# Kernel tuning notes

Hardware: AMD Instinct MI355X
Metric: run time of the kernel (lower is better)

The kernel has to match this reference:

```python
import jax, jax.numpy as jnp
import numpy as np

N_BINS = 15  # matches init n_bins; bin b covers (b/15, (b+1)/15]


def setup_inputs() -> dict:
    key = jax.random.key(0)
    k1, k2 = jax.random.split(key)
    N, C = 500000, 100
    logits = jax.random.normal(k1, (N, C), dtype=jnp.float32)
    labels = jax.random.randint(k2, (N,), 0, C)
    return {"logits": logits, "labels": labels}


def reference(logits, labels):
    n_bins = N_BINS
    N, C = logits.shape  # num_classes = labels.max()+1 == C w.h.p. for this data
    p = jax.nn.softmax(logits, axis=1)  # [N, C] class confidences
    # Original bin test: p > lower and p <= upper with boundaries linspace(0,1,n_bins+1)
    # => bin index = ceil(p * n_bins) - 1 (exact boundary values fall in the lower bin).
    bin_idx = jnp.clip(jnp.ceil(p * n_bins).astype(jnp.int32) - 1, 0, n_bins - 1)  # [N, C]
    # Flatten to a single segmented histogram over class*n_bins + bin.
    seg = (jnp.arange(C, dtype=jnp.int32)[None, :] * n_bins + bin_idx).reshape(-1)  # [N*C]
    conf = p.reshape(-1)
    correct = (labels[:, None] == jnp.arange(C)[None, :]).astype(p.dtype).reshape(-1)
    num_seg = C * n_bins
    cnt = jax.ops.segment_sum(jnp.ones_like(conf), seg, num_segments=num_seg)
    conf_sum = jax.ops.segment_sum(conf, seg, num_segments=num_seg)
    acc_sum = jax.ops.segment_sum(correct, seg, num_segments=num_seg)
    safe_cnt = jnp.maximum(cnt, 1.0)
    gap = jnp.abs(conf_sum / safe_cnt - acc_sum / safe_cnt)  # |avg_conf - acc| per (class,bin)
    prop = cnt / N  # prop_in_bin (each class column has N entries)
    per_bin = jnp.where(cnt > 0, gap * prop, 0.0)
    per_class_sce = per_bin.reshape(C, n_bins).sum(axis=1)  # [C]
    return per_class_sce.mean()
```

## Files before the change

### kernel.cpp

```cpp
#include <hip/hip_runtime.h>
#include <math.h>

#define NBINS 15
#define NCLS  100
#define NHALF 50
#define NSEG  (NBINS * NCLS)
#define R     4

template <int CTRL>
__device__ __forceinline__ float dpp_add_f32(float x) {
    int y = __builtin_amdgcn_update_dpp(0, __float_as_int(x), CTRL, 0xf, 0xf, true);
    return x + __int_as_float(y);
}
__device__ __forceinline__ float wave_sum64(float x) {
    x = dpp_add_f32<0x111>(x);
    x = dpp_add_f32<0x112>(x);
    x = dpp_add_f32<0x114>(x);
    x = dpp_add_f32<0x118>(x);
    x = dpp_add_f32<0x142>(x);
    x = dpp_add_f32<0x143>(x);
    return __int_as_float(__builtin_amdgcn_readlane(__float_as_int(x), 63));
}

__global__ __launch_bounds__(1024, 8)
void ece_hist(const float* __restrict__ logits,
              const int* __restrict__ labels,
              int N,
              double* __restrict__ g_conf,
              unsigned int* __restrict__ g_acc)
{
    __shared__ float        s_conf[NSEG];
    __shared__ unsigned int s_acc[NSEG];

    const int tid = threadIdx.x;
    for (int i = tid; i < NSEG; i += 1024) { s_conf[i] = 0.0f; s_acc[i] = 0u; }
    __syncthreads();

    const int  lane = tid & 63;
    const int  wv   = (blockIdx.x << 4) + (tid >> 6);
    const int  nwv  = gridDim.x << 4;
    const bool act  = lane < NHALF;

    float        conf0_a = 0.0f, conf0_b = 0.0f;
    unsigned int acc0_a  = 0u,   acc0_b  = 0u;

    const float2* base2 = reinterpret_cast<const float2*>(logits);

    for (int row0 = wv * R; row0 < N; row0 += nwv * R) {
        const bool full = (row0 + R <= N);
        float e0[R], e1[R], s[R];
        int   lbl[R];

        const float2* rp = base2 + (size_t)row0 * NHALF + lane;
        if (full) {
            #pragma unroll
            for (int r = 0; r < R; ++r) {
                float2 v = act ? rp[r * NHALF] : make_float2(0.0f, 0.0f);
                e0[r] = v.x; e1[r] = v.y;
            }
            int4 lb = *reinterpret_cast<const int4*>(labels + row0);
            lbl[0] = lb.x; lbl[1] = lb.y; lbl[2] = lb.z; lbl[3] = lb.w;
        } else {
            #pragma unroll
            for (int r = 0; r < R; ++r) {
                int row = min(row0 + r, N - 1);
                float2 v = act ? base2[(size_t)row * NHALF + lane] : make_float2(0.0f, 0.0f);
                e0[r] = v.x; e1[r] = v.y;
                lbl[r] = labels[row];
            }
        }

        #pragma unroll
        for (int r = 0; r < R; ++r) {
            e0[r] = act ? __expf(e0[r]) : 0.0f;
            e1[r] = act ? __expf(e1[r]) : 0.0f;
        }

        #pragma unroll
        for (int r = 0; r < R; ++r) s[r] = wave_sum64(e0[r] + e1[r]);

        #pragma unroll
        for (int r = 0; r < R; ++r) {
            if (!full && row0 + r >= N) break;
            const float inv    = __builtin_amdgcn_rcpf(s[r]);
            const float thresh = s[r] * (1.0f / (float)NBINS);
            const int   lb     = lbl[r];
            const bool  mine   = (lane == (lb >> 1));
            const int   lbbit  = lb & 1;

            {
                float p0 = e0[r] * inv;
                if (e0[r] > thresh) {
                    int b0 = min((int)ceilf(p0 * (float)NBINS) - 1, NBINS - 1);
                    atomicAdd(&s_conf[(2 * lane) * NBINS + b0], p0);
                    if (mine && lbbit == 0) atomicAdd(&s_acc[(2 * lane) * NBINS + b0], 1u);
                } else {
                    conf0_a += p0;
                    if (mine && lbbit == 0) ++acc0_a;
                }
            }
            {
                float p1 = e1[r] * inv;
                if (e1[r] > thresh) {
                    int b1 = min((int)ceilf(p1 * (float)NBINS) - 1, NBINS - 1);
                    atomicAdd(&s_conf[(2 * lane + 1) * NBINS + b1], p1);
                    if (mine && lbbit == 1) atomicAdd(&s_acc[(2 * lane + 1) * NBINS + b1], 1u);
                } else {
                    conf0_b += p1;
                    if (mine && lbbit == 1) ++acc0_b;
                }
            }
        }
    }

    if (act) {
        atomicAdd(&s_conf[(2 * lane) * NBINS], conf0_a);
        if (acc0_a) atomicAdd(&s_acc[(2 * lane) * NBINS], acc0_a);
        atomicAdd(&s_conf[(2 * lane + 1) * NBINS], conf0_b);
        if (acc0_b) atomicAdd(&s_acc[(2 * lane + 1) * NBINS], acc0_b);
    }

    __syncthreads();
    const int rot = (blockIdx.x * 61) % NSEG;
    for (int i = tid; i < NSEG; i += 1024) {
        int j = i + rot; if (j >= NSEG) j -= NSEG;
        float        c = s_conf[j];
        unsigned int a = s_acc[j];
        if (c != 0.0f) atomicAdd(&g_conf[j], (double)c);
        if (a)         atomicAdd(&g_acc[j], a);
    }
}

__global__ void ece_final(const double* __restrict__ g_conf,
                          const unsigned int* __restrict__ g_acc,
                          float* __restrict__ out, double inv_nc)
{
    __shared__ double sh[16];
    double t = 0.0;
    for (int i = threadIdx.x; i < NSEG; i += blockDim.x)
        t += fabs(g_conf[i] - (double)g_acc[i]);
    #pragma unroll
    for (int off = 32; off; off >>= 1) t += __shfl_xor(t, off);
    const int lane = threadIdx.x & 63, w = threadIdx.x >> 6;
    if (lane == 0) sh[w] = t;
    __syncthreads();
    if (threadIdx.x == 0) {
        double tot = 0.0;
        const int nw = (int)(blockDim.x >> 6);
        for (int i = 0; i < nw; ++i) tot += sh[i];
        out[0] = (float)(tot * inv_nc);
    }
}

extern "C" void kernel_launch(void* const* d_in, const int* in_sizes, int n_in,
                              void* d_out, int out_size, void* d_ws, size_t ws_size,
                              hipStream_t stream)
{
    const float* logits = (const float*)d_in[0];
    const int*   labels = (const int*)d_in[1];
    const int N = in_sizes[1];

    double*       g_conf = (double*)d_ws;
    unsigned int* g_acc  = (unsigned int*)(g_conf + NSEG);

    (void)hipMemsetAsync(d_ws, 0, NSEG * sizeof(double) + NSEG * sizeof(unsigned int), stream);

    ece_hist<<<512, 1024, 0, stream>>>(logits, labels, N, g_conf, g_acc);

    const double inv_nc = 1.0 / ((double)N * (double)NCLS);
    ece_final<<<1, 256, 0, stream>>>(g_conf, g_acc, (float*)d_out, inv_nc);
}
```

Baseline: 58.73 us.

## Fuse final reduction via last-block counter and prefetch next row tile

Merges the separate finalize kernel into the histogram kernel, using a global done counter so the last block computes the final sum. The main loop now software-prefetches the next tile of logits and labels into registers while processing the current one, to hide global load latency. The bin-0 accumulation is restructured to be branchless, and the atomic path is skipped when neither element is rare. In exchange it raises register pressure from double-buffering and adds a threadfence plus a global atomic per block.

```diff
diff --git a/kernel.cpp b/kernel.cpp
--- a/kernel.cpp
+++ b/kernel.cpp
@@ -6,6 +6,8 @@
 #define NHALF 50
 #define NSEG  (NBINS * NCLS)
 #define R     4
+#define NBLK  512
+#define NTHR  1024
 
 template <int CTRL>
 __device__ __forceinline__ float dpp_add_f32(float x) {
@@ -22,18 +24,42 @@
     return __int_as_float(__builtin_amdgcn_readlane(__float_as_int(x), 63));
 }
 
-__global__ __launch_bounds__(1024, 8)
-void ece_hist(const float* __restrict__ logits,
-              const int* __restrict__ labels,
-              int N,
-              double* __restrict__ g_conf,
-              unsigned int* __restrict__ g_acc)
+__device__ __forceinline__ void load_tile(const float2* __restrict__ base2,
+                                          const int* __restrict__ labels,
+                                          int r0, int N, bool act, int lane,
+                                          float2 (&b)[R], int (&lb)[R])
+{
+    if (r0 + R <= N) {
+        const float2* rp = base2 + (size_t)r0 * NHALF + lane;
+        #pragma unroll
+        for (int r = 0; r < R; ++r)
+            b[r] = act ? rp[r * NHALF] : make_float2(0.0f, 0.0f);
+        const int4 l4 = *reinterpret_cast<const int4*>(labels + r0);
+        lb[0] = l4.x; lb[1] = l4.y; lb[2] = l4.z; lb[3] = l4.w;
+    } else {
+        #pragma unroll
+        for (int r = 0; r < R; ++r) {
+            int row = min(r0 + r, N - 1);
+            b[r] = act ? base2[(size_t)row * NHALF + lane] : make_float2(0.0f, 0.0f);
+            lb[r] = labels[row];
+        }
+    }
+}
+
+__global__ __launch_bounds__(NTHR, 8)
+void ece_fused(const float* __restrict__ logits,
+               const int* __restrict__ labels,
+               int N,
+               double* __restrict__ g_conf,
+               unsigned int* __restrict__ g_acc,
+               unsigned int* __restrict__ g_done,
+               float* __restrict__ out, double inv_nc)
 {
     __shared__ float        s_conf[NSEG];
     __shared__ unsigned int s_acc[NSEG];
 
     const int tid = threadIdx.x;
-    for (int i = tid; i < NSEG; i += 1024) { s_conf[i] = 0.0f; s_acc[i] = 0u; }
+    for (int i = tid; i < NSEG; i += NTHR) { s_conf[i] = 0.0f; s_acc[i] = 0u; }
     __syncthreads();
 
     const int  lane = tid & 63;
@@ -44,73 +70,67 @@
     float        conf0_a = 0.0f, conf0_b = 0.0f;
     unsigned int acc0_a  = 0u,   acc0_b  = 0u;
 
-    const float2* base2 = reinterpret_cast<const float2*>(logits);
+    const float2* base2  = reinterpret_cast<const float2*>(logits);
+    const int     stride = nwv * R;
 
-    for (int row0 = wv * R; row0 < N; row0 += nwv * R) {
-        const bool full = (row0 + R <= N);
-        float e0[R], e1[R], s[R];
-        int   lbl[R];
+    int row0 = wv * R;
+    float2 cbuf[R]; int clbl[R];
+    if (row0 < N) load_tile(base2, labels, row0, N, act, lane, cbuf, clbl);
 
-        const float2* rp = base2 + (size_t)row0 * NHALF + lane;
-        if (full) {
-            #pragma unroll
-            for (int r = 0; r < R; ++r) {
-                float2 v = act ? rp[r * NHALF] : make_float2(0.0f, 0.0f);
-                e0[r] = v.x; e1[r] = v.y;
-            }
-            int4 lb = *reinterpret_cast<const int4*>(labels + row0);
-            lbl[0] = lb.x; lbl[1] = lb.y; lbl[2] = lb.z; lbl[3] = lb.w;
-        } else {
-            #pragma unroll
-            for (int r = 0; r < R; ++r) {
-                int row = min(row0 + r, N - 1);
-                float2 v = act ? base2[(size_t)row * NHALF + lane] : make_float2(0.0f, 0.0f);
-                e0[r] = v.x; e1[r] = v.y;
-                lbl[r] = labels[row];
-            }
+    while (row0 < N) {
+        const int nrow0 = row0 + stride;
+        float2 nbuf[R]; int nlbl[R];
+        if (nrow0 < N)
+            load_tile(base2, labels, nrow0, N, act, lane, nbuf, nlbl);
+
+        float e0[R], e1[R], s[R], invv[R], th[R];
+        #pragma unroll
+        for (int r = 0; r < R; ++r) {
+            e0[r] = act ? __expf(cbuf[r].x) : 0.0f;
+            e1[r] = act ? __expf(cbuf[r].y) : 0.0f;
+        }
+        #pragma unroll
+        for (int r = 0; r < R; ++r) s[r] = wave_sum64(e0[r] + e1[r]);
+        #pragma unroll
+        for (int r = 0; r < R; ++r) {
+            invv[r] = __builtin_amdgcn_rcpf(s[r]);
+            th[r]   = s[r] * (1.0f / (float)NBINS);
         }
 
         #pragma unroll
         for (int r = 0; r < R; ++r) {
-            e0[r] = act ? __expf(e0[r]) : 0.0f;
-            e1[r] = act ? __expf(e1[r]) : 0.0f;
-        }
-
-        #pragma unroll
-        for (int r = 0; r < R; ++r) s[r] = wave_sum64(e0[r] + e1[r]);
-
-        #pragma unroll
-        for (int r = 0; r < R; ++r) {
-            if (!full && row0 + r >= N) break;
-            const float inv    = __builtin_amdgcn_rcpf(s[r]);
-            const float thresh = s[r] * (1.0f / (float)NBINS);
-            const int   lb     = lbl[r];
-            const bool  mine   = (lane == (lb >> 1));
-            const int   lbbit  = lb & 1;
-
-            {
-                float p0 = e0[r] * inv;
-                if (e0[r] > thresh) {
-                    int b0 = min((int)ceilf(p0 * (float)NBINS) - 1, NBINS - 1);
+            if (row0 + r >= N) break;
+            const float p0 = e0[r] * invv[r];
+            const float p1 = e1[r] * invv[r];
+            const bool  rare0 = e0[r] > th[r];
+            const bool  rare1 = e1[r] > th[r];
+            conf0_a += rare0 ? 0.0f : p0;
+            conf0_b += rare1 ? 0.0f : p1;
+            const int  lb   = clbl[r];
+            const bool mine = (lane == (lb >> 1));
+            if (mine) {
+                if (lb & 1) { if (!rare1) ++acc0_b; }
+                else        { if (!rare0) ++acc0_a; }
+            }
+            if (rare0 | rare1) {
+                if (rare0) {
+                    const int b0 = min((int)ceilf(p0 * (float)NBINS) - 1, NBINS - 1);
                     atomicAdd(&s_conf[(2 * lane) * NBINS + b0], p0);
-                    if (mine && lbbit == 0) atomicAdd(&s_acc[(2 * lane) * NBINS + b0], 1u);
-                } else {
-                    conf0_a += p0;
-                    if (mine && lbbit == 0) ++acc0_a;
+                    if (mine && !(lb & 1)) atomicAdd(&s_acc[(2 * lane) * NBINS + b0], 1u);
                 }
-            }
-            {
-                float p1 = e1[r] * inv;
-                if (e1[r] > thresh) {
-                    int b1 = min((int)ceilf(p1 * (float)NBINS) - 1, NBINS - 1);
+                if (rare1) {
+                    const int b1 = min((int)ceilf(p1 * (float)NBINS) - 1, NBINS - 1);
                     atomicAdd(&s_conf[(2 * lane + 1) * NBINS + b1], p1);
-                    if (mine && lbbit == 1) atomicAdd(&s_acc[(2 * lane + 1) * NBINS + b1], 1u);
-                } else {
-                    conf0_b += p1;
-                    if (mine && lbbit == 1) ++acc0_b;
+                    if (mine && (lb & 1)) atomicAdd(&s_acc[(2 * lane + 1) * NBINS + b1], 1u);
                 }
             }
         }
+
+        if (nrow0 < N) {
+            #pragma unroll
+            for (int r = 0; r < R; ++r) { cbuf[r] = nbuf[r]; clbl[r] = nlbl[r]; }
+        }
+        row0 = nrow0;
     }
 
     if (act) {
@@ -122,33 +142,36 @@
 
     __syncthreads();
     const int rot = (blockIdx.x * 61) % NSEG;
-    for (int i = tid; i < NSEG; i += 1024) {
+    for (int i = tid; i < NSEG; i += NTHR) {
         int j = i + rot; if (j >= NSEG) j -= NSEG;
         float        c = s_conf[j];
         unsigned int a = s_acc[j];
         if (c != 0.0f) atomicAdd(&g_conf[j], (double)c);
         if (a)         atomicAdd(&g_acc[j], a);
     }
-}
 
-__global__ void ece_final(const double* __restrict__ g_conf,
-                          const unsigned int* __restrict__ g_acc,
-                          float* __restrict__ out, double inv_nc)
-{
-    __shared__ double sh[16];
-    double t = 0.0;
-    for (int i = threadIdx.x; i < NSEG; i += blockDim.x)
-        t += fabs(g_conf[i] - (double)g_acc[i]);
-    #pragma unroll
-    for (int off = 32; off; off >>= 1) t += __shfl_xor(t, off);
-    const int lane = threadIdx.x & 63, w = threadIdx.x >> 6;
-    if (lane == 0) sh[w] = t;
+    __threadfence();
+    __shared__ unsigned int s_last;
+    if (tid == 0) s_last = (atomicAdd(g_done, 1u) == gridDim.x - 1) ? 1u : 0u;
     __syncthreads();
-    if (threadIdx.x == 0) {
-        double tot = 0.0;
-        const int nw = (int)(blockDim.x >> 6);
-        for (int i = 0; i < nw; ++i) tot += sh[i];
-        out[0] = (float)(tot * inv_nc);
+    if (s_last) {
+        double t = 0.0;
+        for (int i = tid; i < NSEG; i += NTHR) {
+            double       c = atomicAdd(&g_conf[i], 0.0);
+            unsigned int a = atomicAdd(&g_acc[i], 0u);
+            t += fabs(c - (double)a);
+        }
+        #pragma unroll
+        for (int off = 32; off; off >>= 1) t += __shfl_xor(t, off);
+        __shared__ double sh[16];
+        if ((tid & 63) == 0) sh[tid >> 6] = t;
+        __syncthreads();
+        if (tid == 0) {
+            double tot = 0.0;
+            #pragma unroll
+            for (int i = 0; i < 16; ++i) tot += sh[i];
+            out[0] = (float)(tot * inv_nc);
+        }
     }
 }
 
@@ -162,11 +185,14 @@
 
     double*       g_conf = (double*)d_ws;
     unsigned int* g_acc  = (unsigned int*)(g_conf + NSEG);
+    unsigned int* g_done = g_acc + NSEG;
 
-    (void)hipMemsetAsync(d_ws, 0, NSEG * sizeof(double) + NSEG * sizeof(unsigned int), stream);
-
-    ece_hist<<<512, 1024, 0, stream>>>(logits, labels, N, g_conf, g_acc);
+    (void)hipMemsetAsync(d_ws, 0,
+                         NSEG * sizeof(double) + (NSEG + 1) * sizeof(unsigned int),
+                         stream);
 
     const double inv_nc = 1.0 / ((double)N * (double)NCLS);
-    ece_final<<<1, 256, 0, stream>>>(g_conf, g_acc, (float*)d_out, inv_nc);
+    ece_fused<<<NBLK, NTHR, 0, stream>>>(logits, labels, N,
+                                         g_conf, g_acc, g_done,
+                                         (float*)d_out, inv_nc);
 }
```

After: 177.5 us. 202% more time.

## Stage 128-row logit tiles through LDS with coalesced float4 loads

Applied to the files above, without the earlier changes.

Each block now copies a 128-row tile of logits into shared memory using fully coalesced float4 loads, then each wave reads 8 rows from LDS as float2 pairs. The previous per-wave float2 global loads left 14 of 64 lanes idle. The grid doubles to 1024 blocks. The change adds two block barriers per tile and about 51 KB of LDS per block, which lowers occupancy and removes the overlap between loading and computing inside a block.

```diff
diff --git a/kernel.cpp b/kernel.cpp
--- a/kernel.cpp
+++ b/kernel.cpp
@@ -5,7 +5,8 @@
 #define NCLS  100
 #define NHALF 50
 #define NSEG  (NBINS * NCLS)
-#define R     4
+#define TROWS 128
+#define NF4T  (TROWS * NCLS / 4)
 
 template <int CTRL>
 __device__ __forceinline__ float dpp_add_f32(float x) {
@@ -29,85 +30,102 @@
               double* __restrict__ g_conf,
               unsigned int* __restrict__ g_acc)
 {
+    __shared__ __align__(16) float s_tile[TROWS * NCLS];
     __shared__ float        s_conf[NSEG];
     __shared__ unsigned int s_acc[NSEG];
 
     const int tid = threadIdx.x;
     for (int i = tid; i < NSEG; i += 1024) { s_conf[i] = 0.0f; s_acc[i] = 0u; }
-    __syncthreads();
 
     const int  lane = tid & 63;
-    const int  wv   = (blockIdx.x << 4) + (tid >> 6);
-    const int  nwv  = gridDim.x << 4;
+    const int  w    = tid >> 6;
     const bool act  = lane < NHALF;
 
     float        conf0_a = 0.0f, conf0_b = 0.0f;
     unsigned int acc0_a  = 0u,   acc0_b  = 0u;
 
-    const float2* base2 = reinterpret_cast<const float2*>(logits);
+    const float4* g4 = reinterpret_cast<const float4*>(logits);
+    float4*       t4 = reinterpret_cast<float4*>(s_tile);
+    const float2* s2 = reinterpret_cast<const float2*>(s_tile);
 
-    for (int row0 = wv * R; row0 < N; row0 += nwv * R) {
-        const bool full = (row0 + R <= N);
-        float e0[R], e1[R], s[R];
-        int   lbl[R];
+    const int ntiles = (N + TROWS - 1) / TROWS;
 
-        const float2* rp = base2 + (size_t)row0 * NHALF + lane;
-        if (full) {
-            #pragma unroll
-            for (int r = 0; r < R; ++r) {
-                float2 v = act ? rp[r * NHALF] : make_float2(0.0f, 0.0f);
-                e0[r] = v.x; e1[r] = v.y;
-            }
-            int4 lb = *reinterpret_cast<const int4*>(labels + row0);
-            lbl[0] = lb.x; lbl[1] = lb.y; lbl[2] = lb.z; lbl[3] = lb.w;
-        } else {
-            #pragma unroll
-            for (int r = 0; r < R; ++r) {
-                int row = min(row0 + r, N - 1);
-                float2 v = act ? base2[(size_t)row * NHALF + lane] : make_float2(0.0f, 0.0f);
-                e0[r] = v.x; e1[r] = v.y;
-                lbl[r] = labels[row];
-            }
-        }
+    for (int tile = blockIdx.x; tile < ntiles; tile += gridDim.x) {
+        const int start = tile * TROWS;
+        const int rows  = min(TROWS, N - start);
+        const int nf4   = rows * (NCLS / 4);
+
+        __syncthreads();
+        const size_t gbase = (size_t)start * (NCLS / 4);
+        for (int i = tid; i < nf4; i += 1024)
+            t4[i] = g4[gbase + i];
+        __syncthreads();
 
         #pragma unroll
-        for (int r = 0; r < R; ++r) {
-            e0[r] = act ? __expf(e0[r]) : 0.0f;
-            e1[r] = act ? __expf(e1[r]) : 0.0f;
-        }
+        for (int half = 0; half < 2; ++half) {
+            const int r0 = w * 8 + half * 4;
+            if (r0 >= rows) break;
+            const bool full = (r0 + 4 <= rows);
+            float e0[4], e1[4], s[4];
+            int   lbl[4];
 
-        #pragma unroll
-        for (int r = 0; r < R; ++r) s[r] = wave_sum64(e0[r] + e1[r]);
-
-        #pragma unroll
-        for (int r = 0; r < R; ++r) {
-            if (!full && row0 + r >= N) break;
-            const float inv    = __builtin_amdgcn_rcpf(s[r]);
-            const float thresh = s[r] * (1.0f / (float)NBINS);
-            const int   lb     = lbl[r];
-            const bool  mine   = (lane == (lb >> 1));
-            const int   lbbit  = lb & 1;
-
-            {
-                float p0 = e0[r] * inv;
-                if (e0[r] > thresh) {
-                    int b0 = min((int)ceilf(p0 * (float)NBINS) - 1, NBINS - 1);
-                    atomicAdd(&s_conf[(2 * lane) * NBINS + b0], p0);
-                    if (mine && lbbit == 0) atomicAdd(&s_acc[(2 * lane) * NBINS + b0], 1u);
-                } else {
-                    conf0_a += p0;
-                    if (mine && lbbit == 0) ++acc0_a;
+            if (full) {
+                #pragma unroll
+                for (int r = 0; r < 4; ++r) {
+                    float2 v = act ? s2[(r0 + r) * NHALF + lane] : make_float2(0.f, 0.f);
+                    e0[r] = v.x; e1[r] = v.y;
+                }
+                const int4 lb = *reinterpret_cast<const int4*>(labels + start + r0);
+                lbl[0] = lb.x; lbl[1] = lb.y; lbl[2] = lb.z; lbl[3] = lb.w;
+            } else {
+                #pragma unroll
+                for (int r = 0; r < 4; ++r) {
+                    int rr = min(r0 + r, rows - 1);
+                    float2 v = act ? s2[rr * NHALF + lane] : make_float2(0.f, 0.f);
+                    e0[r] = v.x; e1[r] = v.y;
+                    lbl[r] = labels[start + rr];
                 }
             }
-            {
-                float p1 = e1[r] * inv;
-                if (e1[r] > thresh) {
-                    int b1 = min((int)ceilf(p1 * (float)NBINS) - 1, NBINS - 1);
-                    atomicAdd(&s_conf[(2 * lane + 1) * NBINS + b1], p1);
-                    if (mine && lbbit == 1) atomicAdd(&s_acc[(2 * lane + 1) * NBINS + b1], 1u);
-                } else {
-                    conf0_b += p1;
-                    if (mine && lbbit == 1) ++acc0_b;
+
+            #pragma unroll
+            for (int r = 0; r < 4; ++r) {
+                e0[r] = act ? __expf(e0[r]) : 0.0f;
+                e1[r] = act ? __expf(e1[r]) : 0.0f;
+            }
+
+            #pragma unroll
+            for (int r = 0; r < 4; ++r) s[r] = wave_sum64(e0[r] + e1[r]);
+
+            #pragma unroll
+            for (int r = 0; r < 4; ++r) {
+                if (!full && r0 + r >= rows) break;
+                const float inv    = __builtin_amdgcn_rcpf(s[r]);
+                const float thresh = s[r] * (1.0f / (float)NBINS);
+                const int   lb     = lbl[r];
+                const bool  mine   = (lane == (lb >> 1));
+                const int   lbbit  = lb & 1;
+
+                {
+                    float p0 = e0[r] * inv;
+                    if (e0[r] > thresh) {
+                        int b0 = min((int)ceilf(p0 * (float)NBINS) - 1, NBINS - 1);
+                        atomicAdd(&s_conf[(2 * lane) * NBINS + b0], p0);
+                        if (mine && lbbit == 0) atomicAdd(&s_acc[(2 * lane) * NBINS + b0], 1u);
+                    } else {
+                        conf0_a += p0;
+                        if (mine && lbbit == 0) ++acc0_a;
+                    }
+                }
+                {
+                    float p1 = e1[r] * inv;
+                    if (e1[r] > thresh) {
+                        int b1 = min((int)ceilf(p1 * (float)NBINS) - 1, NBINS - 1);
+                        atomicAdd(&s_conf[(2 * lane + 1) * NBINS + b1], p1);
+                        if (mine && lbbit == 1) atomicAdd(&s_acc[(2 * lane + 1) * NBINS + b1], 1u);
+                    } else {
+                        conf0_b += p1;
+                        if (mine && lbbit == 1) ++acc0_b;
+                    }
                 }
             }
         }
@@ -165,7 +183,7 @@
 
     (void)hipMemsetAsync(d_ws, 0, NSEG * sizeof(double) + NSEG * sizeof(unsigned int), stream);
 
-    ece_hist<<<512, 1024, 0, stream>>>(logits, labels, N, g_conf, g_acc);
+    ece_hist<<<1024, 1024, 0, stream>>>(logits, labels, N, g_conf, g_acc);
 
     const double inv_nc = 1.0 / ((double)N * (double)NCLS);
     ece_final<<<1, 256, 0, stream>>>(g_conf, g_acc, (float*)d_out, inv_nc);
```

After: 79.02 us. 34.5% more time.
